# Optimization experiments

Measured on AMD Instinct MI355X. Metric: run time of the kernel, lower is better.

Reference implementation:

```python
import jax, jax.numpy as jnp
import numpy as np

N = 100000   # nodes
E = 1600000  # edges
F = 128      # num_features
H = 128      # embedding_size
C = 10       # num_classes
G = 64       # graphs in batch


def setup_inputs() -> dict:
    key = jax.random.key(0)
    ks = jax.random.split(key, 10)
    x = jax.random.normal(ks[0], (N, F), jnp.float32)
    edge_index = jax.random.randint(ks[1], (2, E), 0, N)
    batch_index = jnp.sort(jax.random.randint(ks[2], (N,), 0, G))
    glorot = lambda k, shape: jax.random.normal(k, shape, jnp.float32) / np.float32(np.sqrt(shape[0]))
    return {
        "x": x, "edge_index": edge_index, "batch_index": batch_index,
        "W0": glorot(ks[3], (F, H)), "b0": jnp.zeros((H,), jnp.float32),
        "W1": glorot(ks[4], (H, H)), "b1": jnp.zeros((H,), jnp.float32),
        "W2": glorot(ks[5], (H, H)), "b2": jnp.zeros((H,), jnp.float32),
        "W3": glorot(ks[6], (H, H)), "b3": jnp.zeros((H,), jnp.float32),
        "Wout": glorot(ks[7], (2 * H, C)), "bout": jnp.zeros((C,), jnp.float32),
    }


def gcn_conv(x, W, b, src, dst):
    """PyG GCNConv: self-loops + symmetric D^-1/2 (A+I) D^-1/2 normalization."""
    n = x.shape[0]
    # degree with self-loop: deg[i] = 1 + in-degree(i)
    deg = 1.0 + jax.ops.segment_sum(jnp.ones(dst.shape[0], x.dtype), dst, num_segments=n)
    dinv = jax.lax.rsqrt(deg)
    h = x @ W  # [N, H]
    norm = (dinv[src] * dinv[dst])[:, None]  # [E, 1]
    agg = jax.ops.segment_sum(h[src] * norm, dst, num_segments=n)  # scatter-add over edges
    agg = agg + h * (1.0 / deg)[:, None]  # self-loop contribution dinv[i]^2 * h[i]
    return agg + b


def reference(x, edge_index, batch_index, W0, b0, W1, b1, W2, b2, W3, b3, Wout, bout):
    src, dst = edge_index[0], edge_index[1]
    h = jnp.tanh(gcn_conv(x, W0, b0, src, dst))
    h = jnp.tanh(gcn_conv(h, W1, b1, src, dst))
    h = jnp.tanh(gcn_conv(h, W2, b2, src, dst))
    h = jnp.tanh(gcn_conv(h, W3, b3, src, dst))
    # global max pool + global mean pool over batch_index
    gmax = jax.ops.segment_max(h, batch_index, num_segments=G)
    cnt = jax.ops.segment_sum(jnp.ones((h.shape[0],), h.dtype), batch_index, num_segments=G)
    gmean = jax.ops.segment_sum(h, batch_index, num_segments=G) / jnp.maximum(cnt, 1.0)[:, None]
    pooled = jnp.concatenate([gmax, gmean], axis=1)  # [G, 2H]
    out = pooled @ Wout + bout  # [G, C]
    return out, pooled
```

## Files before the change

### kernel.cpp

```cpp
#include <hip/hip_runtime.h>
#include <hip/hip_fp16.h>
#include <cmath>

typedef __attribute__((ext_vector_type(8))) short short8;
typedef __attribute__((ext_vector_type(8))) unsigned short ushort8;
typedef __attribute__((ext_vector_type(8))) _Float16 f16x8;
typedef __attribute__((ext_vector_type(4))) float f32x4;

__device__ __forceinline__ unsigned pk_bf16(float a, float b) {
  unsigned r;
  asm("v_cvt_pk_bf16_f32 %0, %1, %2" : "=v"(r) : "v"(a), "v"(b));
  return r;
}

__device__ __forceinline__ float fast_tanh(float x) {
  float e2 = __expf(2.0f * x);
  return 1.0f - 2.0f * __builtin_amdgcn_rcpf(e2 + 1.0f);
}

#define FM_LO(A, U, W) \
  asm("v_fma_mix_f32 %0, %1, %2, %0 op_sel_hi:[1,0,0]" : "+v"(A) : "v"(U), "v"(W))
#define FM_HI(A, U, W) \
  asm("v_fma_mix_f32 %0, %1, %2, %0 op_sel:[1,0,0] op_sel_hi:[1,0,0]" : "+v"(A) : "v"(U), "v"(W))


__global__ __launch_bounds__(256) void wconv0(const float* __restrict__ W0,
                                              unsigned short* __restrict__ Wt0Hi,
                                              unsigned short* __restrict__ Wt0Lo) {
  int idx = blockIdx.x * 256 + threadIdx.x;
  if (idx >= 8192) return;
  int n = idx & 127, k = (idx >> 7) * 2;
  float w0 = W0[k * 128 + n], w1 = W0[(k + 1) * 128 + n];
  unsigned h01 = pk_bf16(w0, w1);
  float hf0 = __uint_as_float(h01 << 16);
  float hf1 = __uint_as_float(h01 & 0xFFFF0000u);
  unsigned l01 = pk_bf16(w0 - hf0, w1 - hf1);
  *(unsigned*)&Wt0Hi[n * 128 + k] = h01;
  *(unsigned*)&Wt0Lo[n * 128 + k] = l01;
}


__device__ __forceinline__ void gemm0_block(int bx, const float* __restrict__ A,
                                            const unsigned short* __restrict__ WtHi,
                                            const unsigned short* __restrict__ WtLo,
                                            __half* __restrict__ O, int M) {
  int tid = threadIdx.x;
  int wv = tid >> 6, lane = tid & 63;
  int r0 = bx * 128 + wv * 32;
  int lrow = lane & 15, lk = (lane >> 4) * 8;

  f32x4 acc[2][8] = {};
#pragma unroll
  for (int kk = 0; kk < 4; ++kk) {
    int k0 = kk * 32 + lk;
    short8 ahi[2], alo[2];
#pragma unroll
    for (int fr = 0; fr < 2; ++fr) {
      int row = r0 + fr * 16 + lrow;
      row = row < M ? row : M - 1;
      const float* ap = &A[(size_t)row * 128 + k0];
      float4 a0 = *(const float4*)ap;
      float4 a1 = *(const float4*)(ap + 4);
      union { short8 v; unsigned u32[4]; } h_, l_;
#define SPLIT2(slot, x, y)                              \
      {                                                 \
        unsigned hh = pk_bf16((x), (y));                \
        h_.u32[slot] = hh;                              \
        float hf0 = __uint_as_float(hh << 16);          \
        float hf1 = __uint_as_float(hh & 0xFFFF0000u);  \
        l_.u32[slot] = pk_bf16((x) - hf0, (y) - hf1);   \
      }
      SPLIT2(0, a0.x, a0.y)
      SPLIT2(1, a0.z, a0.w)
      SPLIT2(2, a1.x, a1.y)
      SPLIT2(3, a1.z, a1.w)
#undef SPLIT2
      ahi[fr] = h_.v;
      alo[fr] = l_.v;
    }
#pragma unroll
    for (int c = 0; c < 8; ++c) {
      int bidx = (c * 16 + lrow) * 128 + k0;
      short8 bhi = *(const short8*)&WtHi[bidx];
      short8 blo = *(const short8*)&WtLo[bidx];
#pragma unroll
      for (int fr = 0; fr < 2; ++fr) {
        acc[fr][c] = __builtin_amdgcn_mfma_f32_16x16x32_bf16(ahi[fr], bhi, acc[fr][c], 0, 0, 0);
        acc[fr][c] = __builtin_amdgcn_mfma_f32_16x16x32_bf16(ahi[fr], blo, acc[fr][c], 0, 0, 0);
        acc[fr][c] = __builtin_amdgcn_mfma_f32_16x16x32_bf16(alo[fr], bhi, acc[fr][c], 0, 0, 0);
      }
    }
  }
#pragma unroll
  for (int fr = 0; fr < 2; ++fr) {
#pragma unroll
    for (int c = 0; c < 8; ++c) {
#pragma unroll
      for (int r = 0; r < 4; ++r) {
        int row = r0 + fr * 16 + (lane >> 4) * 4 + r;
        if (row < M)
          O[(size_t)row * 128 + c * 16 + (lane & 15)] = __float2half(acc[fr][c][r]);
      }
    }
  }
}


__global__ __launch_bounds__(256) void mega_a(
    const int* __restrict__ dst, int* __restrict__ cnt, int* __restrict__ epos,
    int E, int ncnt, int ngemm, int p,
    const float* __restrict__ W1, const float* __restrict__ W2,
    const float* __restrict__ W3, unsigned short* __restrict__ WfHi,
    unsigned short* __restrict__ WfLo,
    const float* __restrict__ x, const unsigned short* __restrict__ Wt0Hi,
    const unsigned short* __restrict__ Wt0Lo, __half* __restrict__ bufA, int M) {
  int bid = blockIdx.x;
  int g = bid / p;
  if ((bid % p) == 0 && g < ngemm) {
    gemm0_block(g, x, Wt0Hi, Wt0Lo, bufA, M);
    return;
  }
  int before = (g < ngemm) ? (g + 1) : ngemm;
  int other = bid - before;
  if (other < ncnt) {
    int e = other * 256 + threadIdx.x;
    if (e < E) epos[e] = atomicAdd(&cnt[dst[e]], 1);
    return;
  }
  int t = (other - ncnt) * 256 + threadIdx.x;
  int l = 1 + (t >> 13);
  int idx = t & 8191;
  const float* W = (l == 1) ? W1 : (l == 2) ? W2 : W3;
  int n = idx & 127, k = (idx >> 7) * 2;
  float w0 = W[k * 128 + n], w1 = W[(k + 1) * 128 + n];
  __half2 hh = __float22half2_rn(make_float2(w0, w1));
  float r0 = __low2float(hh), r1 = __high2float(hh);
  __half2 ll = __float22half2_rn(make_float2((w0 - r0) * 1024.0f,
                                             (w1 - r1) * 1024.0f));
  *(__half2*)&WfHi[(l - 1) * 16384 + n * 128 + k] = hh;
  *(__half2*)&WfLo[(l - 1) * 16384 + n * 128 + k] = ll;
}


__global__ __launch_bounds__(512) void scan_a(const int* __restrict__ cnt,
                                              int* __restrict__ rs,
                                              int* __restrict__ bsum,
                                              float* __restrict__ dinv,
                                              float* __restrict__ dinv2, int n) {
  __shared__ int s[512];
  int tid = threadIdx.x;
  int gid = blockIdx.x * 512 + tid;
  int v = (gid < n) ? cnt[gid] : 0;
  if (gid < n) {
    float deg = 1.0f + (float)v;
    dinv[gid] = rsqrtf(deg);
    dinv2[gid] = __builtin_amdgcn_rcpf(deg);
  }
  s[tid] = v;
  __syncthreads();
  for (int off = 1; off < 512; off <<= 1) {
    int t = (tid >= off) ? s[tid - off] : 0;
    __syncthreads();
    s[tid] += t;
    __syncthreads();
  }
  if (gid < n) rs[gid] = s[tid] - v;
  if (tid == 511) bsum[blockIdx.x] = s[511];
}

__global__ __launch_bounds__(256) void scan_b(const int* __restrict__ bsum,
                                              int* __restrict__ boff, int nb,
                                              const int* __restrict__ batch,
                                              int* __restrict__ gstart, int n,
                                              int G) {
  __shared__ int s[256];
  int tid = threadIdx.x;
  int v = (tid < nb) ? bsum[tid] : 0;
  s[tid] = v;
  __syncthreads();
  for (int off = 1; off < 256; off <<= 1) {
    int t = (tid >= off) ? s[tid - off] : 0;
    __syncthreads();
    s[tid] += t;
    __syncthreads();
  }
  if (tid < nb) boff[tid] = s[tid] - v;
  if (tid <= G) {
    int lo = 0, hi = n;
    while (lo < hi) {
      int mid = (lo + hi) >> 1;
      if (batch[mid] < tid) lo = mid + 1;
      else hi = mid;
    }
    gstart[tid] = lo;
  }
}

__global__ __launch_bounds__(512) void scan_c(const int* __restrict__ boff,
                                              int* __restrict__ rs, int n, int E) {
  int gid = blockIdx.x * 512 + threadIdx.x;
  if (gid < n) rs[gid] += boff[blockIdx.x];
  if (gid == 0) rs[n] = E;
}


__global__ __launch_bounds__(256) void fill_k(const int* __restrict__ src,
                                              const int* __restrict__ dst,
                                              const int* __restrict__ rs,
                                              const int* __restrict__ epos,
                                              const float* __restrict__ dinv,
                                              int2* __restrict__ edata, int E) {
  int e = blockIdx.x * 256 + threadIdx.x;
  if (e >= E) return;
  int s = src[e], d = dst[e];
  int pos = rs[d] + epos[e];
  int2 ed;
  ed.x = s;
  ed.y = __float_as_int(dinv[s] * dinv[d]);
  edata[pos] = ed;
}


#define LDK 136

__global__ __launch_bounds__(256) void gemm_f16(const __half* __restrict__ Hf,
                                                const unsigned short* __restrict__ Whi,
                                                const unsigned short* __restrict__ Wlo,
                                                __half* __restrict__ O, int M) {
  __shared__ unsigned short sHi[128 * LDK];
  __shared__ unsigned short sLo[128 * LDK];
  int tid = threadIdx.x;
#pragma unroll
  for (int i = 0; i < 8; ++i) {
    int c = tid + i * 256;
    int n = c >> 4;
    int off = (c & 15) * 8;
    *(ushort8*)&sHi[n * LDK + off] = *(const ushort8*)&Whi[c * 8];
    *(ushort8*)&sLo[n * LDK + off] = *(const ushort8*)&Wlo[c * 8];
  }
  __syncthreads();

  int wv = tid >> 6, lane = tid & 63;
  int r0 = blockIdx.x * 128 + wv * 32;
  int lrow = lane & 15, lk = (lane >> 4) * 8;

  f32x4 acc[2][8] = {};
  f32x4 accL[2][8] = {};
#pragma unroll
  for (int kk = 0; kk < 4; ++kk) {
    int k0 = kk * 32 + lk;
    f16x8 a[2];
#pragma unroll
    for (int fr = 0; fr < 2; ++fr) {
      int row = r0 + fr * 16 + lrow;
      row = row < M ? row : M - 1;
      a[fr] = *(const f16x8*)&Hf[(size_t)row * 128 + k0];
    }
#pragma unroll
    for (int c = 0; c < 8; ++c) {
      int bidx = (c * 16 + lrow) * LDK + k0;
      f16x8 bhi = *(const f16x8*)&sHi[bidx];
      f16x8 blo = *(const f16x8*)&sLo[bidx];
#pragma unroll
      for (int fr = 0; fr < 2; ++fr) {
        acc[fr][c] = __builtin_amdgcn_mfma_f32_16x16x32_f16(a[fr], bhi, acc[fr][c], 0, 0, 0);
        accL[fr][c] = __builtin_amdgcn_mfma_f32_16x16x32_f16(a[fr], blo, accL[fr][c], 0, 0, 0);
      }
    }
  }
  const float ls = 1.0f / 1024.0f;
#pragma unroll
  for (int fr = 0; fr < 2; ++fr) {
#pragma unroll
    for (int c = 0; c < 8; ++c) {
#pragma unroll
      for (int r = 0; r < 4; ++r) {
        int row = r0 + fr * 16 + (lane >> 4) * 4 + r;
        if (row < M)
          O[(size_t)row * 128 + c * 16 + (lane & 15)] =
              __float2half(acc[fr][c][r] + accL[fr][c][r] * ls);
      }
    }
  }
}


__global__ __launch_bounds__(256) void gather_k(const __half* __restrict__ h,
                                                const int* __restrict__ rs,
                                                const int2* __restrict__ edata,
                                                const float* __restrict__ dinv2,
                                                const float* __restrict__ bias,
                                                __half* __restrict__ Hf, int N) {
  int wid = (int)((blockIdx.x * (size_t)blockDim.x + threadIdx.x) >> 6);
  if (wid >= N) return;
  int lane = threadIdx.x & 63;
  int grp = lane >> 4;
  int li = lane & 15;
  int s = rs[wid], e = rs[wid + 1];
  const uint4* hrow = (const uint4*)h;
  const unsigned long long* ed64 = (const unsigned long long*)edata;

  float ac[8] = {};
  int niter = (e - s + 15) >> 4;
  int base = s + grp;
#define ACC(U, W)                                        \
  {                                                      \
    FM_LO(ac[0], (U).x, (W)); FM_HI(ac[1], (U).x, (W));  \
    FM_LO(ac[2], (U).y, (W)); FM_HI(ac[3], (U).y, (W));  \
    FM_LO(ac[4], (U).z, (W)); FM_HI(ac[5], (U).z, (W));  \
    FM_LO(ac[6], (U).w, (W)); FM_HI(ac[7], (U).w, (W));  \
  }
  for (int it = 0; it < niter; ++it, base += 16) {
    int p0 = base, p1 = base + 4, p2 = base + 8, p3 = base + 12;
    int c0 = p0 < e ? p0 : s, c1 = p1 < e ? p1 : s;
    int c2 = p2 < e ? p2 : s, c3 = p3 < e ? p3 : s;
    unsigned long long u0 = __builtin_nontemporal_load(&ed64[c0]);
    unsigned long long u1 = __builtin_nontemporal_load(&ed64[c1]);
    unsigned long long u2 = __builtin_nontemporal_load(&ed64[c2]);
    unsigned long long u3 = __builtin_nontemporal_load(&ed64[c3]);
    unsigned i0 = (unsigned)u0, i1 = (unsigned)u1;
    unsigned i2 = (unsigned)u2, i3 = (unsigned)u3;
    float w0 = p0 < e ? __uint_as_float((unsigned)(u0 >> 32)) : 0.0f;
    float w1 = p1 < e ? __uint_as_float((unsigned)(u1 >> 32)) : 0.0f;
    float w2 = p2 < e ? __uint_as_float((unsigned)(u2 >> 32)) : 0.0f;
    float w3 = p3 < e ? __uint_as_float((unsigned)(u3 >> 32)) : 0.0f;
    uint4 v0 = hrow[(size_t)i0 * 16 + li];
    uint4 v1 = hrow[(size_t)i1 * 16 + li];
    uint4 v2 = hrow[(size_t)i2 * 16 + li];
    uint4 v3 = hrow[(size_t)i3 * 16 + li];
    ACC(v0, w0) ACC(v1, w1) ACC(v2, w2) ACC(v3, w3)
  }
#undef ACC
#pragma unroll
  for (int j = 0; j < 8; ++j) {
    ac[j] += __shfl_xor(ac[j], 16);
    ac[j] += __shfl_xor(ac[j], 32);
  }

  float a0 = grp == 0 ? ac[0] : grp == 1 ? ac[2] : grp == 2 ? ac[4] : ac[6];
  float a1 = grp == 0 ? ac[1] : grp == 1 ? ac[3] : grp == 2 ? ac[5] : ac[7];

  float d2 = dinv2[wid];
  uint4 sv = hrow[(size_t)wid * 16 + li];
  unsigned su = grp == 0 ? sv.x : grp == 1 ? sv.y : grp == 2 ? sv.z : sv.w;
  float2 sj = __half22float2(*(__half2*)&su);
  float2 bj = *(const float2*)&bias[li * 8 + 2 * grp];
  float o0 = fast_tanh(a0 + sj.x * d2 + bj.x);
  float o1 = fast_tanh(a1 + sj.y * d2 + bj.y);

  __half2 hv = __float22half2_rn(make_float2(o0, o1));
  *(__half2*)&Hf[(size_t)wid * 128 + li * 8 + 2 * grp] = hv;
}


#define CH 16

__global__ __launch_bounds__(128) void pool_partial(const __half* __restrict__ Hf,
                                                    const int* __restrict__ gstart,
                                                    float* __restrict__ pmax,
                                                    float* __restrict__ psum) {
  int g = blockIdx.x, c = blockIdx.y, f = threadIdx.x;
  int s = gstart[g], e = gstart[g + 1];
  long long len = e - s;
  int cs = s + (int)(len * c / CH);
  int ce = s + (int)(len * (c + 1) / CH);
  float m = -INFINITY, sum = 0.f;
  for (int n = cs; n < ce; ++n) {
    float v = __half2float(Hf[(size_t)n * 128 + f]);
    m = fmaxf(m, v);
    sum += v;
  }
  pmax[((size_t)g * CH + c) * 128 + f] = m;
  psum[((size_t)g * CH + c) * 128 + f] = sum;
}

__global__ __launch_bounds__(128) void pool_head(const float* __restrict__ pmax,
                                                 const float* __restrict__ psum,
                                                 const int* __restrict__ gstart,
                                                 const float* __restrict__ Wout,
                                                 const float* __restrict__ bout,
                                                 float* __restrict__ out, int G) {
  __shared__ float pl[256];
  int g = blockIdx.x, f = threadIdx.x;
  float m = -INFINITY, s = 0.f;
  for (int c = 0; c < CH; ++c) {
    m = fmaxf(m, pmax[((size_t)g * CH + c) * 128 + f]);
    s += psum[((size_t)g * CH + c) * 128 + f];
  }
  int cnt = gstart[g + 1] - gstart[g];
  float mean = s / fmaxf((float)cnt, 1.0f);
  float* pooled = out + (size_t)G * 10;
  pooled[(size_t)g * 256 + f] = m;
  pooled[(size_t)g * 256 + 128 + f] = mean;
  pl[f] = m;
  pl[128 + f] = mean;
  __syncthreads();
  if (f < 10) {
    float acc = bout[f];
    for (int k = 0; k < 256; ++k) acc += pl[k] * Wout[k * 10 + f];
    out[(size_t)g * 10 + f] = acc;
  }
}


extern "C" void kernel_launch(void* const* d_in, const int* in_sizes, int n_in,
                              void* d_out, int out_size, void* d_ws, size_t ws_size,
                              hipStream_t stream) {
  const float* x = (const float*)d_in[0];
  const int* ei = (const int*)d_in[1];
  const int* batch = (const int*)d_in[2];
  const float* W[4] = {(const float*)d_in[3], (const float*)d_in[5],
                       (const float*)d_in[7], (const float*)d_in[9]};
  const float* Bz[4] = {(const float*)d_in[4], (const float*)d_in[6],
                        (const float*)d_in[8], (const float*)d_in[10]};
  const float* Wout = (const float*)d_in[11];
  const float* bout = (const float*)d_in[12];
  const int N = in_sizes[0] / 128;
  const int E = in_sizes[1] / 2;
  const int G = 64;
  const int* srcp = ei;
  const int* dstp = ei + E;
  float* out = (float*)d_out;

  char* wsb = (char*)d_ws;
  size_t off = 0;
  auto alloc = [&](size_t bytes) -> void* {
    void* p = wsb + off;
    off = (off + bytes + 255) & ~(size_t)255;
    return p;
  };
  __half* bufA = (__half*)alloc((size_t)N * 128 * 2);
  __half* Hf = (__half*)alloc((size_t)N * 128 * 2);
  size_t cnt_off = off;
  int* cnt = (int*)alloc((size_t)N * 4);
  size_t cnt_span = off - cnt_off;
  int* epos = (int*)alloc((size_t)E * 4);
  float* dinv = (float*)alloc((size_t)N * 4);
  float* dinv2 = (float*)alloc((size_t)N * 4);
  int* rs = (int*)alloc((size_t)(N + 1) * 4);
  int2* edata = (int2*)alloc((size_t)E * 8);
  int* bsum = (int*)alloc(4096);
  int* boff = (int*)alloc(4096);
  int* gstart = (int*)alloc(4096);
  float* pmax = (float*)alloc((size_t)G * CH * 128 * 4);
  float* psum = (float*)alloc((size_t)G * CH * 128 * 4);
  unsigned short* Wt0Hi = (unsigned short*)alloc(16384 * 2);
  unsigned short* Wt0Lo = (unsigned short*)alloc(16384 * 2);
  unsigned short* WfHi = (unsigned short*)alloc(3 * 16384 * 2);
  unsigned short* WfLo = (unsigned short*)alloc(3 * 16384 * 2);
  if (off > ws_size) return;

  hipMemsetAsync(wsb + cnt_off, 0, cnt_span, stream);

  wconv0<<<32, 256, 0, stream>>>(W[0], Wt0Hi, Wt0Lo);

  int ncnt = (E + 255) / 256;
  int ngemm = (N + 127) / 128;
  int total = ncnt + 96 + ngemm;
  int p = total / ngemm;
  mega_a<<<total, 256, 0, stream>>>(dstp, cnt, epos, E, ncnt, ngemm, p, W[1],
                                    W[2], W[3], WfHi, WfLo, x, Wt0Hi, Wt0Lo,
                                    bufA, N);

  int nsb = (N + 511) / 512;
  scan_a<<<nsb, 512, 0, stream>>>(cnt, rs, bsum, dinv, dinv2, N);
  scan_b<<<1, 256, 0, stream>>>(bsum, boff, nsb, batch, gstart, N, G);
  scan_c<<<nsb, 512, 0, stream>>>(boff, rs, N, E);
  fill_k<<<(E + 255) / 256, 256, 0, stream>>>(srcp, dstp, rs, epos, dinv, edata, E);

  int ggrid = (int)(((size_t)N * 64 + 255) / 256);
  for (int l = 0; l < 4; ++l) {
    if (l > 0)
      gemm_f16<<<(N + 127) / 128, 256, 0, stream>>>(Hf, WfHi + (l - 1) * 16384,
                                                    WfLo + (l - 1) * 16384, bufA, N);
    gather_k<<<ggrid, 256, 0, stream>>>(bufA, rs, edata, dinv2, Bz[l], Hf, N);
  }

  pool_partial<<<dim3(G, CH), 128, 0, stream>>>(Hf, gstart, pmax, psum);
  pool_head<<<G, 128, 0, stream>>>(pmax, psum, gstart, Wout, bout, out, G);
}
```

Before: 515.9 us.

## Drop scan_c by folding block offsets into consumers; shrink gemm0 tiles

The scan_c kernel, which added per-block prefix offsets to the row-start array, is removed. fill_k and gather_k now add boff[d>>9] on the fly, and gather_k uses E for the final row end. Separately, the layer-0 GEMM fused into mega_a now processes 64 rows per block (16 per wave) instead of 128, doubling the gemm block count, with launch_bounds minimum 6 blocks per SM to lower register pressure and raise occupancy. This saves one launch and one pass over rs, at the cost of an extra small load per edge and per node in each gather layer, and less A/B reuse in the GEMM.

```diff
diff --git a/kernel.cpp b/kernel.cpp
--- a/kernel.cpp
+++ b/kernel.cpp
@@ -46,67 +46,56 @@
                                             __half* __restrict__ O, int M) {
   int tid = threadIdx.x;
   int wv = tid >> 6, lane = tid & 63;
-  int r0 = bx * 128 + wv * 32;
+  int r0 = bx * 64 + wv * 16;
   int lrow = lane & 15, lk = (lane >> 4) * 8;
 
-  f32x4 acc[2][8] = {};
+  f32x4 acc[8] = {};
 #pragma unroll
   for (int kk = 0; kk < 4; ++kk) {
     int k0 = kk * 32 + lk;
-    short8 ahi[2], alo[2];
-#pragma unroll
-    for (int fr = 0; fr < 2; ++fr) {
-      int row = r0 + fr * 16 + lrow;
-      row = row < M ? row : M - 1;
-      const float* ap = &A[(size_t)row * 128 + k0];
-      float4 a0 = *(const float4*)ap;
-      float4 a1 = *(const float4*)(ap + 4);
-      union { short8 v; unsigned u32[4]; } h_, l_;
+    int row = r0 + lrow;
+    row = row < M ? row : M - 1;
+    const float* ap = &A[(size_t)row * 128 + k0];
+    float4 a0 = *(const float4*)ap;
+    float4 a1 = *(const float4*)(ap + 4);
+    union { short8 v; unsigned u32[4]; } h_, l_;
 #define SPLIT2(slot, x, y)                              \
-      {                                                 \
-        unsigned hh = pk_bf16((x), (y));                \
-        h_.u32[slot] = hh;                              \
-        float hf0 = __uint_as_float(hh << 16);          \
-        float hf1 = __uint_as_float(hh & 0xFFFF0000u);  \
-        l_.u32[slot] = pk_bf16((x) - hf0, (y) - hf1);   \
-      }
-      SPLIT2(0, a0.x, a0.y)
-      SPLIT2(1, a0.z, a0.w)
-      SPLIT2(2, a1.x, a1.y)
-      SPLIT2(3, a1.z, a1.w)
+    {                                                   \
+      unsigned hh = pk_bf16((x), (y));                  \
+      h_.u32[slot] = hh;                                \
+      float hf0 = __uint_as_float(hh << 16);            \
+      float hf1 = __uint_as_float(hh & 0xFFFF0000u);    \
+      l_.u32[slot] = pk_bf16((x) - hf0, (y) - hf1);     \
+    }
+    SPLIT2(0, a0.x, a0.y)
+    SPLIT2(1, a0.z, a0.w)
+    SPLIT2(2, a1.x, a1.y)
+    SPLIT2(3, a1.z, a1.w)
 #undef SPLIT2
-      ahi[fr] = h_.v;
-      alo[fr] = l_.v;
-    }
+    short8 ahi = h_.v, alo = l_.v;
 #pragma unroll
     for (int c = 0; c < 8; ++c) {
       int bidx = (c * 16 + lrow) * 128 + k0;
       short8 bhi = *(const short8*)&WtHi[bidx];
       short8 blo = *(const short8*)&WtLo[bidx];
-#pragma unroll
-      for (int fr = 0; fr < 2; ++fr) {
-        acc[fr][c] = __builtin_amdgcn_mfma_f32_16x16x32_bf16(ahi[fr], bhi, acc[fr][c], 0, 0, 0);
-        acc[fr][c] = __builtin_amdgcn_mfma_f32_16x16x32_bf16(ahi[fr], blo, acc[fr][c], 0, 0, 0);
-        acc[fr][c] = __builtin_amdgcn_mfma_f32_16x16x32_bf16(alo[fr], bhi, acc[fr][c], 0, 0, 0);
-      }
-    }
-  }
-#pragma unroll
-  for (int fr = 0; fr < 2; ++fr) {
-#pragma unroll
-    for (int c = 0; c < 8; ++c) {
-#pragma unroll
-      for (int r = 0; r < 4; ++r) {
-        int row = r0 + fr * 16 + (lane >> 4) * 4 + r;
-        if (row < M)
-          O[(size_t)row * 128 + c * 16 + (lane & 15)] = __float2half(acc[fr][c][r]);
-      }
-    }
-  }
-}
-
-
-__global__ __launch_bounds__(256) void mega_a(
+      acc[c] = __builtin_amdgcn_mfma_f32_16x16x32_bf16(ahi, bhi, acc[c], 0, 0, 0);
+      acc[c] = __builtin_amdgcn_mfma_f32_16x16x32_bf16(ahi, blo, acc[c], 0, 0, 0);
+      acc[c] = __builtin_amdgcn_mfma_f32_16x16x32_bf16(alo, bhi, acc[c], 0, 0, 0);
+    }
+  }
+#pragma unroll
+  for (int c = 0; c < 8; ++c) {
+#pragma unroll
+    for (int r = 0; r < 4; ++r) {
+      int row = r0 + (lane >> 4) * 4 + r;
+      if (row < M)
+        O[(size_t)row * 128 + c * 16 + (lane & 15)] = __float2half(acc[c][r]);
+    }
+  }
+}
+
+
+__global__ __launch_bounds__(256, 6) void mega_a(
     const int* __restrict__ dst, int* __restrict__ cnt, int* __restrict__ epos,
     int E, int ncnt, int ngemm, int p,
     const float* __restrict__ W1, const float* __restrict__ W2,
@@ -196,24 +185,18 @@
   }
 }
 
-__global__ __launch_bounds__(512) void scan_c(const int* __restrict__ boff,
-                                              int* __restrict__ rs, int n, int E) {
-  int gid = blockIdx.x * 512 + threadIdx.x;
-  if (gid < n) rs[gid] += boff[blockIdx.x];
-  if (gid == 0) rs[n] = E;
-}
-
 
 __global__ __launch_bounds__(256) void fill_k(const int* __restrict__ src,
                                               const int* __restrict__ dst,
                                               const int* __restrict__ rs,
+                                              const int* __restrict__ boff,
                                               const int* __restrict__ epos,
                                               const float* __restrict__ dinv,
                                               int2* __restrict__ edata, int E) {
   int e = blockIdx.x * 256 + threadIdx.x;
   if (e >= E) return;
   int s = src[e], d = dst[e];
-  int pos = rs[d] + epos[e];
+  int pos = rs[d] + boff[d >> 9] + epos[e];
   int2 ed;
   ed.x = s;
   ed.y = __float_as_int(dinv[s] * dinv[d]);
@@ -287,16 +270,19 @@
 
 __global__ __launch_bounds__(256) void gather_k(const __half* __restrict__ h,
                                                 const int* __restrict__ rs,
+                                                const int* __restrict__ boff,
                                                 const int2* __restrict__ edata,
                                                 const float* __restrict__ dinv2,
                                                 const float* __restrict__ bias,
-                                                __half* __restrict__ Hf, int N) {
+                                                __half* __restrict__ Hf, int N,
+                                                int E) {
   int wid = (int)((blockIdx.x * (size_t)blockDim.x + threadIdx.x) >> 6);
   if (wid >= N) return;
   int lane = threadIdx.x & 63;
   int grp = lane >> 4;
   int li = lane & 15;
-  int s = rs[wid], e = rs[wid + 1];
+  int s = rs[wid] + boff[wid >> 9];
+  int e = (wid + 1 < N) ? (rs[wid + 1] + boff[(wid + 1) >> 9]) : E;
   const uint4* hrow = (const uint4*)h;
   const unsigned long long* ed64 = (const unsigned long long*)edata;
 
@@ -455,9 +441,10 @@
   wconv0<<<32, 256, 0, stream>>>(W[0], Wt0Hi, Wt0Lo);
 
   int ncnt = (E + 255) / 256;
-  int ngemm = (N + 127) / 128;
+  int ngemm = (N + 63) / 64;
   int total = ncnt + 96 + ngemm;
   int p = total / ngemm;
+  if (p < 1) p = 1;
   mega_a<<<total, 256, 0, stream>>>(dstp, cnt, epos, E, ncnt, ngemm, p, W[1],
                                     W[2], W[3], WfHi, WfLo, x, Wt0Hi, Wt0Lo,
                                     bufA, N);
@@ -465,15 +452,16 @@
   int nsb = (N + 511) / 512;
   scan_a<<<nsb, 512, 0, stream>>>(cnt, rs, bsum, dinv, dinv2, N);
   scan_b<<<1, 256, 0, stream>>>(bsum, boff, nsb, batch, gstart, N, G);
-  scan_c<<<nsb, 512, 0, stream>>>(boff, rs, N, E);
-  fill_k<<<(E + 255) / 256, 256, 0, stream>>>(srcp, dstp, rs, epos, dinv, edata, E);
+  fill_k<<<(E + 255) / 256, 256, 0, stream>>>(srcp, dstp, rs, boff, epos, dinv,
+                                              edata, E);
 
   int ggrid = (int)(((size_t)N * 64 + 255) / 256);
   for (int l = 0; l < 4; ++l) {
     if (l > 0)
       gemm_f16<<<(N + 127) / 128, 256, 0, stream>>>(Hf, WfHi + (l - 1) * 16384,
                                                     WfLo + (l - 1) * 16384, bufA, N);
-    gather_k<<<ggrid, 256, 0, stream>>>(bufA, rs, edata, dinv2, Bz[l], Hf, N);
+    gather_k<<<ggrid, 256, 0, stream>>>(bufA, rs, boff, edata, dinv2, Bz[l], Hf,
+                                        N, E);
   }
 
   pool_partial<<<dim3(G, CH), 128, 0, stream>>>(Hf, gstart, pmax, psum);
```

Measured after the change: 545.9 us. 1.06x slower.
